# Kernel optimization log

Measured on AMD Instinct MI355X. Metric: run time of the kernel, lower is better.

The kernel has to match this reference:

```python
import jax, jax.numpy as jnp
import numpy as np

N = 50000
E = 800000
IN_DIM = 128
OUT_DIM = 64
ALPHA = 0.2  # LeakyReLU negative slope


def setup_inputs() -> dict:
    key = jax.random.key(0)
    k1, k2, k3, k4 = jax.random.split(key, 4)
    x = jax.random.normal(k1, (N, IN_DIM), dtype=jnp.float32)
    # xavier-ish scaled params
    W = jax.random.normal(k2, (IN_DIM, OUT_DIM), dtype=jnp.float32) * (1.0 / np.sqrt(IN_DIM))
    a = jax.random.normal(k3, (2 * OUT_DIM, 1), dtype=jnp.float32) * (1.0 / np.sqrt(2 * OUT_DIM))
    edge_index = jax.random.randint(k4, (2, E), 0, N, dtype=jnp.int32)
    return {"x": x, "W": W, "a": a, "edge_index": edge_index}


def reference(x, W, a, edge_index):
    # dropout is inference-mode (identity)
    h = x @ W                                  # [N, out_dim]
    src, dst = edge_index[0], edge_index[1]
    # edge score: leakyrelu(concat(h[src], h[dst]) @ a)
    # = leakyrelu(h[src] @ a[:d] + h[dst] @ a[d:]) -- compute node-level first
    a_src = (h @ a[:OUT_DIM]).squeeze(-1)      # [N]
    a_dst = (h @ a[OUT_DIM:]).squeeze(-1)      # [N]
    e = jax.nn.leaky_relu(a_src[src] + a_dst[dst], negative_slope=ALPHA)  # [E]
    # NOTE: original does F.softmax(edge_e.squeeze(), dim=0) -> GLOBAL softmax over all edges
    att = jax.nn.softmax(e)                    # [E]
    # h_prime[r] = sum_{e: src[e]==r} att[e] * h[dst[e]]
    msgs = att[:, None] * h[dst]               # [E, out_dim]
    h_prime = jax.ops.segment_sum(msgs, src, num_segments=N)  # [N, out_dim]
    return jax.nn.elu(h_prime)
```

## Files before the change

kernel.cpp:

```cpp
#include <hip/hip_runtime.h>
#include <hip/hip_bf16.h>
#include <math.h>

#define N_NODES 50000
#define N_EDGES 800000
#define IN_DIM_ 128
#define OUT_DIM_ 64
#define ALPHA_ 0.2f
#define CAP 64
#define OVF_CAP 8192

__global__ __launch_bounds__(256, 4) void gemm_h(const float* __restrict__ x,
                                                 const float* __restrict__ W,
                                                 const float* __restrict__ a_g,
                                                 float* __restrict__ h,
                                                 float* __restrict__ a_srcv,
                                                 float* __restrict__ a_dstv) {
    __shared__ float At[64][68];
    __shared__ float Wl[64][68];
    const int tid = threadIdx.x;
    const int tx = tid & 15;
    const int ty = tid >> 4;
    const int row0 = blockIdx.x * 64;

    float acc[4][4] = {};

    for (int ks = 0; ks < 128; ks += 64) {
        {
            const int r  = tid >> 4;
            const int k4 = tid & 15;
            #pragma unroll
            for (int rr = 0; rr < 64; rr += 16) {
                const int row = row0 + r + rr;
                float4 v = make_float4(0.f, 0.f, 0.f, 0.f);
                if (row < N_NODES)
                    v = *(const float4*)&x[(size_t)row * IN_DIM_ + ks + k4 * 4];
                At[k4 * 4 + 0][r + rr] = v.x;
                At[k4 * 4 + 1][r + rr] = v.y;
                At[k4 * 4 + 2][r + rr] = v.z;
                At[k4 * 4 + 3][r + rr] = v.w;
            }
            const int kr = tid >> 4;
            const int c4 = tid & 15;
            #pragma unroll
            for (int kk = 0; kk < 64; kk += 16) {
                float4 wv = *(const float4*)&W[(size_t)(ks + kr + kk) * OUT_DIM_ + c4 * 4];
                *(float4*)&Wl[kr + kk][c4 * 4] = wv;
            }
        }
        __syncthreads();

        #pragma unroll 16
        for (int kk = 0; kk < 64; ++kk) {
            const float4 a4 = *(const float4*)&At[kk][ty * 4];
            const float4 b4 = *(const float4*)&Wl[kk][tx * 4];
            acc[0][0] += a4.x * b4.x; acc[0][1] += a4.x * b4.y; acc[0][2] += a4.x * b4.z; acc[0][3] += a4.x * b4.w;
            acc[1][0] += a4.y * b4.x; acc[1][1] += a4.y * b4.y; acc[1][2] += a4.y * b4.z; acc[1][3] += a4.y * b4.w;
            acc[2][0] += a4.z * b4.x; acc[2][1] += a4.z * b4.y; acc[2][2] += a4.z * b4.z; acc[2][3] += a4.z * b4.w;
            acc[3][0] += a4.w * b4.x; acc[3][1] += a4.w * b4.y; acc[3][2] += a4.w * b4.z; acc[3][3] += a4.w * b4.w;
        }
        __syncthreads();
    }

    const float a0 = a_g[tx * 4 + 0], a1 = a_g[tx * 4 + 1];
    const float a2 = a_g[tx * 4 + 2], a3 = a_g[tx * 4 + 3];
    const float b0 = a_g[64 + tx * 4 + 0], b1 = a_g[64 + tx * 4 + 1];
    const float b2 = a_g[64 + tx * 4 + 2], b3 = a_g[64 + tx * 4 + 3];

    #pragma unroll
    for (int i = 0; i < 4; ++i) {
        const int row = row0 + ty * 4 + i;
        if (row < N_NODES) {
            float4 o = make_float4(acc[i][0], acc[i][1], acc[i][2], acc[i][3]);
            *(float4*)&h[(size_t)row * OUT_DIM_ + tx * 4] = o;
        }
        float s = acc[i][0] * a0 + acc[i][1] * a1 + acc[i][2] * a2 + acc[i][3] * a3;
        float d = acc[i][0] * b0 + acc[i][1] * b1 + acc[i][2] * b2 + acc[i][3] * b3;
        #pragma unroll
        for (int m = 1; m < 16; m <<= 1) {
            s += __shfl_xor(s, m);
            d += __shfl_xor(d, m);
        }
        if (tx == 0 && row < N_NODES) {
            a_srcv[row] = s;
            a_dstv[row] = d;
        }
    }
}

__global__ __launch_bounds__(256) void bucket(const int* __restrict__ ei,
                                              const float* __restrict__ a_srcv,
                                              const float* __restrict__ a_dstv,
                                              int* __restrict__ cnt,
                                              int* __restrict__ edst,
                                              int* __restrict__ ovf_cnt,
                                              int2* __restrict__ ovf,
                                              float* __restrict__ Z) {
    const int e = blockIdx.x * 256 + threadIdx.x;
    float val = 0.f;
    if (e < N_EDGES) {
        const int s = ei[e];
        const int d = ei[N_EDGES + e];
        float t = a_srcv[s] + a_dstv[d];
        t = t > 0.f ? t : ALPHA_ * t;
        val = __expf(t);
        const int slot = atomicAdd(&cnt[s], 1);
        if (slot < CAP) {
            edst[(size_t)s * CAP + slot] = d;
        } else {
            const int o = atomicAdd(ovf_cnt, 1);
            if (o < OVF_CAP) ovf[o] = make_int2(s, d);
        }
    }
    __shared__ float red[4];
    float sum = val;
    #pragma unroll
    for (int m = 32; m; m >>= 1) sum += __shfl_xor(sum, m);
    if ((threadIdx.x & 63) == 0) red[threadIdx.x >> 6] = sum;
    __syncthreads();
    if (threadIdx.x == 0) atomicAdd(Z, red[0] + red[1] + red[2] + red[3]);
}

__global__ __launch_bounds__(256) void accum(const int* __restrict__ cnt,
                                             const int* __restrict__ edst,
                                             const float* __restrict__ a_srcv,
                                             const float* __restrict__ a_dstv,
                                             const float* __restrict__ h,
                                             float* __restrict__ out) {
    const int lane = threadIdx.x & 63;
    const int n = blockIdx.x * 4 + (threadIdx.x >> 6);
    if (n >= N_NODES) return;
    const int deg = min(cnt[n], CAP);
    const float asn = a_srcv[n];
    const int* __restrict__ my = edst + (size_t)n * CAP;

    float acc = 0.f;
    int j = 0;
    for (; j + 4 <= deg; j += 4) {
        const int d0 = my[j + 0], d1 = my[j + 1], d2 = my[j + 2], d3 = my[j + 3];
        float t0 = asn + a_dstv[d0];
        float t1 = asn + a_dstv[d1];
        float t2 = asn + a_dstv[d2];
        float t3 = asn + a_dstv[d3];
        t0 = t0 > 0.f ? t0 : ALPHA_ * t0;
        t1 = t1 > 0.f ? t1 : ALPHA_ * t1;
        t2 = t2 > 0.f ? t2 : ALPHA_ * t2;
        t3 = t3 > 0.f ? t3 : ALPHA_ * t3;
        const float v0 = __expf(t0), v1 = __expf(t1), v2 = __expf(t2), v3 = __expf(t3);
        acc += v0 * h[(size_t)d0 * OUT_DIM_ + lane];
        acc += v1 * h[(size_t)d1 * OUT_DIM_ + lane];
        acc += v2 * h[(size_t)d2 * OUT_DIM_ + lane];
        acc += v3 * h[(size_t)d3 * OUT_DIM_ + lane];
    }
    for (; j < deg; ++j) {
        const int d = my[j];
        float t = asn + a_dstv[d];
        t = t > 0.f ? t : ALPHA_ * t;
        acc += __expf(t) * h[(size_t)d * OUT_DIM_ + lane];
    }
    out[(size_t)n * OUT_DIM_ + lane] = acc;
}

__global__ __launch_bounds__(256) void ovf_fix(const int* __restrict__ ovf_cnt,
                                               const int2* __restrict__ ovf,
                                               const float* __restrict__ a_srcv,
                                               const float* __restrict__ a_dstv,
                                               const float* __restrict__ h,
                                               float* __restrict__ out) {
    const int nov = min(*ovf_cnt, OVF_CAP);
    const int lane = threadIdx.x & 63;
    const int wid = (blockIdx.x * 256 + threadIdx.x) >> 6;
    const int nw = (gridDim.x * 256) >> 6;
    for (int i = wid; i < nov; i += nw) {
        const int2 sd = ovf[i];
        float t = a_srcv[sd.x] + a_dstv[sd.y];
        t = t > 0.f ? t : ALPHA_ * t;
        const float val = __expf(t);
        atomicAdd(&out[(size_t)sd.x * OUT_DIM_ + lane], val * h[(size_t)sd.y * OUT_DIM_ + lane]);
    }
}

__global__ __launch_bounds__(256) void finalize(float* __restrict__ out,
                                                const float* __restrict__ Z) {
    const float inv = 1.0f / *Z;
    const int total4 = N_NODES * OUT_DIM_ / 4;
    const int stride = gridDim.x * 256;
    for (int idx = blockIdx.x * 256 + threadIdx.x; idx < total4; idx += stride) {
        float4 v = ((float4*)out)[idx];
        float u;
        u = v.x * inv; v.x = u > 0.f ? u : expm1f(u);
        u = v.y * inv; v.y = u > 0.f ? u : expm1f(u);
        u = v.z * inv; v.z = u > 0.f ? u : expm1f(u);
        u = v.w * inv; v.w = u > 0.f ? u : expm1f(u);
        ((float4*)out)[idx] = v;
    }
}

extern "C" void kernel_launch(void* const* d_in, const int* in_sizes, int n_in,
                              void* d_out, int out_size, void* d_ws, size_t ws_size,
                              hipStream_t stream) {
    const float* x  = (const float*)d_in[0];
    const float* W  = (const float*)d_in[1];
    const float* a  = (const float*)d_in[2];
    const int*   ei = (const int*)d_in[3];
    float* out = (float*)d_out;

    float* ws     = (float*)d_ws;
    float* h      = ws;
    float* a_srcv = h + (size_t)N_NODES * OUT_DIM_;
    float* a_dstv = a_srcv + N_NODES;
    int*   edst   = (int*)(a_dstv + N_NODES);
    int2*  ovf    = (int2*)(edst + (size_t)N_NODES * CAP);
    int*   cnt    = (int*)(ovf + OVF_CAP);
    float* Z      = (float*)(cnt + N_NODES);
    int*   ovfc   = (int*)(Z + 1);

    hipMemsetAsync(cnt, 0, (size_t)N_NODES * sizeof(int) + 2 * sizeof(int), stream);

    gemm_h<<<(N_NODES + 63) / 64, 256, 0, stream>>>(x, W, a, h, a_srcv, a_dstv);
    bucket<<<(N_EDGES + 255) / 256, 256, 0, stream>>>(ei, a_srcv, a_dstv, cnt, edst, ovfc, ovf, Z);
    accum<<<(N_NODES + 3) / 4, 256, 0, stream>>>(cnt, edst, a_srcv, a_dstv, h, out);
    ovf_fix<<<32, 256, 0, stream>>>(ovfc, ovf, a_srcv, a_dstv, h, out);
    finalize<<<1024, 256, 0, stream>>>(out, Z);
}
```

Measured before the change: 197.8 us.

## Replace per-node edge buckets with 64-node partition bins and LDS accumulation

```diff
diff --git a/kernel.cpp b/kernel.cpp
--- a/kernel.cpp
+++ b/kernel.cpp
@@ -7,7 +7,13 @@
 #define IN_DIM_ 128
 #define OUT_DIM_ 64
 #define ALPHA_ 0.2f
-#define CAP 64
+
+#define PSH 6
+#define PNODES 64
+#define NPART 782
+#define CAPP 2048
+#define BIN_BLOCKS 256
+#define BIN_CHUNK ((N_EDGES + BIN_BLOCKS - 1) / BIN_BLOCKS)
 #define OVF_CAP 8192
 
 __global__ __launch_bounds__(256, 4) void gemm_h(const float* __restrict__ x,
@@ -88,77 +94,106 @@
     }
 }
 
-__global__ __launch_bounds__(256) void bucket(const int* __restrict__ ei,
-                                              const float* __restrict__ a_srcv,
-                                              const float* __restrict__ a_dstv,
-                                              int* __restrict__ cnt,
-                                              int* __restrict__ edst,
-                                              int* __restrict__ ovf_cnt,
-                                              int2* __restrict__ ovf,
-                                              float* __restrict__ Z) {
-    const int e = blockIdx.x * 256 + threadIdx.x;
-    float val = 0.f;
-    if (e < N_EDGES) {
+__global__ __launch_bounds__(256) void bin_edges(const int* __restrict__ ei,
+                                                 int* __restrict__ part_cnt,
+                                                 unsigned int* __restrict__ part_buf,
+                                                 int* __restrict__ ovf_cnt,
+                                                 int2* __restrict__ ovf) {
+    __shared__ int hist[NPART];
+    __shared__ int cur[NPART];
+    const int tid = threadIdx.x;
+    const int e0 = blockIdx.x * BIN_CHUNK;
+    const int e1 = min(e0 + BIN_CHUNK, N_EDGES);
+
+    for (int p = tid; p < NPART; p += 256) hist[p] = 0;
+    __syncthreads();
+
+    for (int e = e0 + tid; e < e1; e += 256) {
+        atomicAdd(&hist[ei[e] >> PSH], 1);
+    }
+    __syncthreads();
+
+    for (int p = tid; p < NPART; p += 256) {
+        const int c = hist[p];
+        cur[p] = (c > 0) ? atomicAdd(&part_cnt[p], c) : 0;
+    }
+    __syncthreads();
+
+    for (int e = e0 + tid; e < e1; e += 256) {
         const int s = ei[e];
         const int d = ei[N_EDGES + e];
-        float t = a_srcv[s] + a_dstv[d];
-        t = t > 0.f ? t : ALPHA_ * t;
-        val = __expf(t);
-        const int slot = atomicAdd(&cnt[s], 1);
-        if (slot < CAP) {
-            edst[(size_t)s * CAP + slot] = d;
+        const int p = s >> PSH;
+        const int slot = atomicAdd(&cur[p], 1);
+        if (slot < CAPP) {
+            part_buf[(size_t)p * CAPP + slot] =
+                ((unsigned)(s & (PNODES - 1)) << 16) | (unsigned)d;
         } else {
             const int o = atomicAdd(ovf_cnt, 1);
             if (o < OVF_CAP) ovf[o] = make_int2(s, d);
         }
     }
-    __shared__ float red[4];
-    float sum = val;
+}
+
+__global__ __launch_bounds__(256) void gather_accum(const int* __restrict__ part_cnt,
+                                                    const unsigned int* __restrict__ part_buf,
+                                                    const float* __restrict__ a_srcv,
+                                                    const float* __restrict__ a_dstv,
+                                                    const float* __restrict__ h,
+                                                    float* __restrict__ out,
+                                                    float* __restrict__ Z) {
+    __shared__ float accs[PNODES][PNODES];
+    __shared__ float asl[PNODES];
+    __shared__ float zred[4];
+    const int p = blockIdx.x;
+    const int tid = threadIdx.x;
+    const int lane = tid & 63;
+    const int wid = tid >> 6;
+    const int n0 = p << PSH;
+
+    float4* az = (float4*)&accs[0][0];
+    for (int i = tid; i < PNODES * PNODES / 4; i += 256)
+        az[i] = make_float4(0.f, 0.f, 0.f, 0.f);
+    if (tid < PNODES)
+        asl[tid] = (n0 + tid < N_NODES) ? a_srcv[n0 + tid] : 0.f;
+    __syncthreads();
+
+    const int cnt = min(part_cnt[p], CAPP);
+    const unsigned int* __restrict__ buf = part_buf + (size_t)p * CAPP;
+    float zacc = 0.f;
+
+    for (int g0 = wid * 64; g0 < cnt; g0 += 4 * 64) {
+        const int i = g0 + lane;
+        const bool valid = i < cnt;
+        const unsigned entry = valid ? buf[i] : 0u;
+        const int d  = entry & 0xFFFFu;
+        const int sl = entry >> 16;
+        float t = asl[sl] + a_dstv[d];
+        t = t > 0.f ? t : ALPHA_ * t;
+        const float w = valid ? __expf(t) : 0.f;
+        zacc += w;
+        #pragma unroll 8
+        for (int j = 0; j < 64; ++j) {
+            const float wj = __shfl(w, j);
+            const int   dj = __shfl(d, j);
+            const int   sj = __shfl(sl, j);
+            const float hv = h[(size_t)dj * OUT_DIM_ + lane];
+            atomicAdd(&accs[sj][lane], wj * hv);
+        }
+    }
+
     #pragma unroll
-    for (int m = 32; m; m >>= 1) sum += __shfl_xor(sum, m);
-    if ((threadIdx.x & 63) == 0) red[threadIdx.x >> 6] = sum;
-    __syncthreads();
-    if (threadIdx.x == 0) atomicAdd(Z, red[0] + red[1] + red[2] + red[3]);
-}
-
-__global__ __launch_bounds__(256) void accum(const int* __restrict__ cnt,
-                                             const int* __restrict__ edst,
-                                             const float* __restrict__ a_srcv,
-                                             const float* __restrict__ a_dstv,
-                                             const float* __restrict__ h,
-                                             float* __restrict__ out) {
-    const int lane = threadIdx.x & 63;
-    const int n = blockIdx.x * 4 + (threadIdx.x >> 6);
-    if (n >= N_NODES) return;
-    const int deg = min(cnt[n], CAP);
-    const float asn = a_srcv[n];
-    const int* __restrict__ my = edst + (size_t)n * CAP;
-
-    float acc = 0.f;
-    int j = 0;
-    for (; j + 4 <= deg; j += 4) {
-        const int d0 = my[j + 0], d1 = my[j + 1], d2 = my[j + 2], d3 = my[j + 3];
-        float t0 = asn + a_dstv[d0];
-        float t1 = asn + a_dstv[d1];
-        float t2 = asn + a_dstv[d2];
-        float t3 = asn + a_dstv[d3];
-        t0 = t0 > 0.f ? t0 : ALPHA_ * t0;
-        t1 = t1 > 0.f ? t1 : ALPHA_ * t1;
-        t2 = t2 > 0.f ? t2 : ALPHA_ * t2;
-        t3 = t3 > 0.f ? t3 : ALPHA_ * t3;
-        const float v0 = __expf(t0), v1 = __expf(t1), v2 = __expf(t2), v3 = __expf(t3);
-        acc += v0 * h[(size_t)d0 * OUT_DIM_ + lane];
-        acc += v1 * h[(size_t)d1 * OUT_DIM_ + lane];
-        acc += v2 * h[(size_t)d2 * OUT_DIM_ + lane];
-        acc += v3 * h[(size_t)d3 * OUT_DIM_ + lane];
-    }
-    for (; j < deg; ++j) {
-        const int d = my[j];
-        float t = asn + a_dstv[d];
-        t = t > 0.f ? t : ALPHA_ * t;
-        acc += __expf(t) * h[(size_t)d * OUT_DIM_ + lane];
-    }
-    out[(size_t)n * OUT_DIM_ + lane] = acc;
+    for (int m = 32; m; m >>= 1) zacc += __shfl_xor(zacc, m);
+    if (lane == 0) zred[wid] = zacc;
+    __syncthreads();
+    if (tid == 0) atomicAdd(Z, zred[0] + zred[1] + zred[2] + zred[3]);
+
+    const int rows_here = min(PNODES, N_NODES - n0);
+    for (int i = tid; i < rows_here * (OUT_DIM_ / 4); i += 256) {
+        const int r  = i >> 4;
+        const int c4 = i & 15;
+        *(float4*)&out[(size_t)(n0 + r) * OUT_DIM_ + c4 * 4] =
+            *(const float4*)&accs[r][c4 * 4];
+    }
 }
 
 __global__ __launch_bounds__(256) void ovf_fix(const int* __restrict__ ovf_cnt,
@@ -205,21 +240,21 @@
     const int*   ei = (const int*)d_in[3];
     float* out = (float*)d_out;
 
-    float* ws     = (float*)d_ws;
-    float* h      = ws;
-    float* a_srcv = h + (size_t)N_NODES * OUT_DIM_;
-    float* a_dstv = a_srcv + N_NODES;
-    int*   edst   = (int*)(a_dstv + N_NODES);
-    int2*  ovf    = (int2*)(edst + (size_t)N_NODES * CAP);
-    int*   cnt    = (int*)(ovf + OVF_CAP);
-    float* Z      = (float*)(cnt + N_NODES);
-    int*   ovfc   = (int*)(Z + 1);
-
-    hipMemsetAsync(cnt, 0, (size_t)N_NODES * sizeof(int) + 2 * sizeof(int), stream);
+    float* ws       = (float*)d_ws;
+    float* h        = ws;
+    float* a_srcv   = h + (size_t)N_NODES * OUT_DIM_;
+    float* a_dstv   = a_srcv + N_NODES;
+    unsigned int* part_buf = (unsigned int*)(a_dstv + N_NODES);
+    int2*  ovf      = (int2*)(part_buf + (size_t)NPART * CAPP);
+    int*   part_cnt = (int*)(ovf + OVF_CAP);
+    float* Z        = (float*)(part_cnt + NPART);
+    int*   ovfc     = (int*)(Z + 1);
+
+    hipMemsetAsync(part_cnt, 0, (NPART + 2) * sizeof(int), stream);
 
     gemm_h<<<(N_NODES + 63) / 64, 256, 0, stream>>>(x, W, a, h, a_srcv, a_dstv);
-    bucket<<<(N_EDGES + 255) / 256, 256, 0, stream>>>(ei, a_srcv, a_dstv, cnt, edst, ovfc, ovf, Z);
-    accum<<<(N_NODES + 3) / 4, 256, 0, stream>>>(cnt, edst, a_srcv, a_dstv, h, out);
+    bin_edges<<<BIN_BLOCKS, 256, 0, stream>>>(ei, part_cnt, part_buf, ovfc, ovf);
+    gather_accum<<<NPART, 256, 0, stream>>>(part_cnt, part_buf, a_srcv, a_dstv, h, out, Z);
     ovf_fix<<<32, 256, 0, stream>>>(ovfc, ovf, a_srcv, a_dstv, h, out);
     finalize<<<1024, 256, 0, stream>>>(out, Z);
 }
```

Measured after the change: 504.4 us. 2.55x slower.
